# Performance work log

Measured on AMD Instinct MI355X. Metric: run time of the kernel, lower is better.

Reference implementation:

```python
import jax, jax.numpy as jnp
import numpy as np

D = 128            # actual_dim / embed_dim
DM = 2 * D         # d_model
HID = 2 * DM       # LSTMCell hidden size
NSYM = 200000
PAD = NSYM
B = 4096
S = 5
NB = 64
STEPS = 4
EPS = 1e-6


def setup_inputs() -> dict:
    key = jax.random.key(0)
    ks = jax.random.split(key, 24)
    def rn(k, sh, scale=0.02):
        return jax.random.normal(k, sh, dtype=jnp.float32) * scale
    emb = rn(ks[10], (NSYM + 1, D)).at[PAD].set(0.0)  # padding row zeroed
    inp = {
        'query': jax.random.randint(ks[0], (B, 2), 0, NSYM),
        'support': jax.random.randint(ks[1], (S, 2), 0, NSYM),
        'q_l_conn': jax.random.randint(ks[2], (B, NB, 2), 0, NSYM),
        'q_l_deg': jax.random.randint(ks[3], (B,), 0, NB),
        'q_r_conn': jax.random.randint(ks[4], (B, NB, 2), 0, NSYM),
        'q_r_deg': jax.random.randint(ks[5], (B,), 0, NB),
        's_l_conn': jax.random.randint(ks[6], (S, NB, 2), 0, NSYM),
        's_l_deg': jax.random.randint(ks[7], (S,), 0, NB),
        's_r_conn': jax.random.randint(ks[8], (S, NB, 2), 0, NSYM),
        's_r_deg': jax.random.randint(ks[9], (S,), 0, NB),
        'emb': emb,
        'gcn_w': rn(ks[11], (D, 2 * D)),
        'gcn_bias': jnp.zeros((D,), jnp.float32),
        'proj1_w': rn(ks[12], (2 * DM, DM)),
        'proj1_b': jnp.zeros((2 * DM,), jnp.float32),
        'proj2_w': rn(ks[13], (DM, 2 * DM)),
        'proj2_b': jnp.zeros((DM,), jnp.float32),
        'ln_g': jnp.ones((DM,), jnp.float32),
        'ln_b': jnp.zeros((DM,), jnp.float32),
        'w_ih': rn(ks[14], (4 * HID, DM)),
        'w_hh': rn(ks[15], (4 * HID, HID)),
        'b_ih': jnp.zeros((4 * HID,), jnp.float32),
        'b_hh': jnp.zeros((4 * HID,), jnp.float32),
    }
    return inp


def _neighbor_encoder(conn, deg, emb, gcn_w, gcn_bias):
    # conn: [N, NB, 2] ids (rel, ent); deg: [N]
    rel = emb[conn[:, :, 0]]                     # [N, NB, D] gather
    ent = emb[conn[:, :, 1]]                     # [N, NB, D] gather
    x = jnp.concatenate([rel, ent], axis=-1)     # [N, NB, 2D]
    out = jnp.einsum('bnd,kd->bnk', x, gcn_w) + gcn_bias  # [N, NB, D]
    denom = jnp.maximum(deg, 1).astype(out.dtype)[:, None]
    return jnp.tanh(out.sum(axis=1) / denom)     # [N, D]


def _support_encoder(x, proj1_w, proj1_b, proj2_w, proj2_b, ln_g, ln_b):
    residual = x
    h = jax.nn.relu(x @ proj1_w.T + proj1_b)
    h = h @ proj2_w.T + proj2_b
    z = h + residual
    mu = z.mean(axis=-1, keepdims=True)
    sigma = jnp.std(z, axis=-1, keepdims=True, ddof=1)
    return ln_g * (z - mu) / (sigma + EPS) + ln_b


def _query_encoder(support_vec, query, w_ih, w_hh, b_ih, b_hh):
    # support_vec: [DM] (single support prototype); query: [B, DM]
    bsz = query.shape[0]
    h_r = jnp.zeros((bsz, HID), query.dtype)
    c = jnp.zeros((bsz, HID), query.dtype)
    xW = query @ w_ih.T + b_ih  # invariant across steps
    h = query
    for _ in range(STEPS):
        gates = xW + h_r @ w_hh.T + b_hh
        i, f, g, o = jnp.split(gates, 4, axis=-1)
        c = jax.nn.sigmoid(f) * c + jax.nn.sigmoid(i) * jnp.tanh(g)
        h_cell = jax.nn.sigmoid(o) * jnp.tanh(c)
        h = query + h_cell[:, :DM]
        # attention over a single support row: softmax of one logit == 1
        r = jnp.broadcast_to(support_vec[None, :], h.shape)
        h_r = jnp.concatenate([h, r], axis=-1)
    return h


def reference(query, support, q_l_conn, q_l_deg, q_r_conn, q_r_deg,
              s_l_conn, s_l_deg, s_r_conn, s_r_deg,
              emb, gcn_w, gcn_bias, proj1_w, proj1_b, proj2_w, proj2_b,
              ln_g, ln_b, w_ih, w_hh, b_ih, b_hh):
    ql = _neighbor_encoder(q_l_conn, q_l_deg, emb, gcn_w, gcn_bias)
    qr = _neighbor_encoder(q_r_conn, q_r_deg, emb, gcn_w, gcn_bias)
    sl = _neighbor_encoder(s_l_conn, s_l_deg, emb, gcn_w, gcn_bias)
    sr = _neighbor_encoder(s_r_conn, s_r_deg, emb, gcn_w, gcn_bias)
    query_nb = jnp.concatenate([ql, qr], axis=-1)    # [B, DM]
    support_nb = jnp.concatenate([sl, sr], axis=-1)  # [S, DM]
    se = lambda x: _support_encoder(x, proj1_w, proj1_b, proj2_w, proj2_b, ln_g, ln_b)
    support_g = se(support_nb).mean(axis=0)          # [DM]
    query_g = se(query_nb)                            # [B, DM]
    query_f = _query_encoder(support_g, query_g, w_ih, w_hh, b_ih, b_hh)
    qn = query_f / jnp.maximum(jnp.linalg.norm(query_f, axis=-1, keepdims=True), 1e-12)
    sn = support_g / jnp.maximum(jnp.linalg.norm(support_g), 1e-12)
    return qn @ sn                                    # [B] matching scores
```

## Files before the change

kernel.cpp:

```cpp
#include <hip/hip_runtime.h>

#define BQ 4096
#define NS 5

typedef __attribute__((ext_vector_type(8))) short bf16x8;
typedef __attribute__((ext_vector_type(4))) float f32x4;
typedef unsigned short ushortT;

#define WS_QNB    0
#define WS_Z      1048576
#define WS_QG     2097152
#define WS_XW     3145728
#define WS_CBUF   7340032
#define WS_H1B    8388608
#define WS_ABF    8912896
#define WS_HB1    9175040
#define WS_P1B    9437184
#define WS_P2B    9502720
#define WS_WIHB   9568256
#define WS_WHHB   9699328
#define WS_GWP    9830400
#define WS_SNB    9863168
#define WS_H1G    9864448
#define WS_ZB     9867008
#define WS_SG     9868288
#define WS_SN     9868544
#define WS_SWL    9868800
#define WS_BL     9869824

__device__ __forceinline__ float wave_allreduce(float v) {
#pragma unroll
  for (int off = 32; off > 0; off >>= 1) v += __shfl_xor(v, off, 64);
  return v;
}
__device__ __forceinline__ float block_allreduce(float v, float* buf) {
  v = wave_allreduce(v);
  __syncthreads();
  if ((threadIdx.x & 63) == 0) buf[threadIdx.x >> 6] = v;
  __syncthreads();
  return buf[0] + buf[1] + buf[2] + buf[3];
}
__device__ __forceinline__ float sigm(float x) { return 1.0f / (1.0f + expf(-x)); }
__device__ __forceinline__ ushortT f2bf(float f) {
  unsigned int u = __float_as_uint(f);
  unsigned int r = (u + 0x7fffu + ((u >> 16) & 1u)) >> 16;
  return (ushortT)r;
}
__device__ __forceinline__ float dot4(float4 a, float4 b) {
  return a.x * b.x + a.y * b.y + a.z * b.z + a.w * b.w;
}

__global__ void k_pack(const float* __restrict__ w_ih, const float* __restrict__ w_hh,
                       const float* __restrict__ p1w, const float* __restrict__ p2w,
                       const float* __restrict__ gcn_w,
                       const float* __restrict__ b_ih, const float* __restrict__ b_hh,
                       ushortT* __restrict__ p1b16, ushortT* __restrict__ p2b16,
                       ushortT* __restrict__ wihb, ushortT* __restrict__ whhb,
                       float4* __restrict__ gwp, float* __restrict__ bL) {
  const int stride = gridDim.x * blockDim.x;
  const int gid = blockIdx.x * blockDim.x + threadIdx.x;
  for (int i = gid; i < 131072; i += stride) p1b16[i] = f2bf(p1w[i]);
  for (int i = gid; i < 131072; i += stride) p2b16[i] = f2bf(p2w[i]);
  for (int i = gid; i < 262144; i += stride) {
    int n = i >> 8, k = i & 255;
    int j = (n >> 2) + 512 * (n & 3);
    wihb[i] = f2bf(w_ih[j * 256 + k]);
    whhb[i] = f2bf(w_hh[j * 512 + k]);
  }
  for (int i = gid; i < 8192; i += stride) {
    int c = i >> 7, k = i & 127;
    const float* s = gcn_w + k * 256 + 4 * c;
    gwp[i] = make_float4(s[0], s[1], s[2], s[3]);
  }
  for (int i = gid; i < 1024; i += stride) {
    int j = (i >> 2) + 512 * (i & 3);
    bL[i] = b_ih[j] + b_hh[j];
  }
}

__global__ __launch_bounds__(256) void k_neighbor(
    const int* __restrict__ qlc, const int* __restrict__ qld,
    const int* __restrict__ qrc, const int* __restrict__ qrd,
    const int* __restrict__ slc, const int* __restrict__ sld,
    const int* __restrict__ src, const int* __restrict__ srd,
    const float* __restrict__ emb, const float4* __restrict__ gwp,
    const float* __restrict__ gcn_bias,
    float* __restrict__ query_nb, float* __restrict__ support_nb,
    ushortT* __restrict__ xq) {
  const int b = blockIdx.x;
  const int t = threadIdx.x;
  const int *cl, *cr;
  int degL, degR;
  float* out;
  if (b < BQ) {
    cl = qlc + b * 128; cr = qrc + b * 128;
    degL = qld[b]; degR = qrd[b];
    out = query_nb + (size_t)b * 256;
  } else {
    int r = b - BQ;
    cl = slc + r * 128; cr = src + r * 128;
    degL = sld[r]; degR = srd[r];
    out = support_nb + (size_t)r * 256;
  }
  __shared__ int conn[256];
  __shared__ __align__(16) float4 xs4[8][32];
  __shared__ __align__(16) float4 xsf[2][64];
  conn[t] = (t < 128) ? cl[t] : cr[t - 128];
  __syncthreads();
  {
    const int side = t >> 7, half = (t >> 6) & 1, ng = (t >> 5) & 1, d4 = t & 31;
    const int* cp = conn + side * 128 + half;
    const float4* emb4 = (const float4*)emb;
    float4 a = make_float4(0.f, 0.f, 0.f, 0.f);
    for (int np = 0; np < 32; np++) {
      int n = 2 * np + ng;
      int idx = cp[2 * n];
      float4 e = emb4[(size_t)idx * 32 + d4];
      a.x += e.x; a.y += e.y; a.z += e.z; a.w += e.w;
    }
    xs4[side * 4 + half * 2 + ng][d4] = a;
  }
  __syncthreads();
  if (t < 128) {
    const int sd = t >> 6, c = t & 63, half = c >> 5, d4 = c & 31;
    float4 a = xs4[sd * 4 + half * 2][d4];
    float4 bb = xs4[sd * 4 + half * 2 + 1][d4];
    a.x += bb.x; a.y += bb.y; a.z += bb.z; a.w += bb.w;
    xsf[sd][c] = a;
  }
  __syncthreads();
  {
    const int sd = t >> 7, kx = t & 127;
    float s = 0.f;
    for (int c = 0; c < 64; c++) s += dot4(gwp[c * 128 + kx], xsf[sd][c]);
    s += 64.0f * gcn_bias[kx];
    int deg = sd ? degR : degL;
    float val = tanhf(s / (float)(deg > 0 ? deg : 1));
    out[sd * 128 + kx] = val;
    if (b < BQ) xq[(size_t)b * 256 + sd * 128 + kx] = f2bf(val);
  }
}

__global__ __launch_bounds__(256) void k_sup1(
    const float* __restrict__ snb, const float* __restrict__ p1w,
    const float* __restrict__ p1b, float* __restrict__ h1g) {
  const int w = blockIdx.x * 4 + (threadIdx.x >> 6);
  const int lane = threadIdx.x & 63;
  const int r = w >> 9, j = w & 511;
  float4 x = *(const float4*)&snb[r * 256 + lane * 4];
  float4 wv = *(const float4*)&p1w[(size_t)j * 256 + lane * 4];
  float s = wave_allreduce(dot4(x, wv));
  if (lane == 0) h1g[r * 512 + j] = fmaxf(s + p1b[j], 0.f);
}

__global__ __launch_bounds__(256) void k_sup2(
    const float* __restrict__ snb, const float* __restrict__ h1g,
    const float* __restrict__ p2w, const float* __restrict__ p2b,
    float* __restrict__ zb) {
  const int w = blockIdx.x * 4 + (threadIdx.x >> 6);
  const int lane = threadIdx.x & 63;
  const int r = w >> 8, tt = w & 255;
  float4 h0 = *(const float4*)&h1g[r * 512 + lane * 4];
  float4 h1 = *(const float4*)&h1g[r * 512 + 256 + lane * 4];
  float4 w0 = *(const float4*)&p2w[(size_t)tt * 512 + lane * 4];
  float4 w1 = *(const float4*)&p2w[(size_t)tt * 512 + 256 + lane * 4];
  float s = wave_allreduce(dot4(h0, w0) + dot4(h1, w1));
  if (lane == 0) zb[r * 256 + tt] = s + p2b[tt] + snb[r * 256 + tt];
}

__global__ __launch_bounds__(256) void k_sup3(
    const float* __restrict__ zb, const float* __restrict__ ln_g,
    const float* __restrict__ ln_b, float* __restrict__ sg, float* __restrict__ sn) {
  const int t = threadIdx.x;
  __shared__ float rbuf[4];
  float acc = 0.f;
  for (int r = 0; r < NS; r++) {
    float z = zb[r * 256 + t];
    float s = block_allreduce(z, rbuf);
    float mu = s * (1.f / 256.f);
    float dz = z - mu;
    float s2 = block_allreduce(dz * dz, rbuf);
    float rstd = 1.f / (sqrtf(s2 * (1.f / 255.f)) + 1e-6f);
    acc += ln_g[t] * dz * rstd + ln_b[t];
    __syncthreads();
  }
  float g = acc * (1.f / (float)NS);
  sg[t] = g;
  float n2 = block_allreduce(g * g, rbuf);
  sn[t] = g / fmaxf(sqrtf(n2), 1e-12f);
}

__global__ __launch_bounds__(256) void k_sup4(
    const float* __restrict__ sg, const float* __restrict__ w_hh,
    float* __restrict__ sWl) {
  const int n = blockIdx.x * 4 + (threadIdx.x >> 6);
  const int lane = threadIdx.x & 63;
  const int j = (n >> 2) + 512 * (n & 3);
  float4 x = *(const float4*)&sg[lane * 4];
  float4 wv = *(const float4*)&w_hh[(size_t)j * 512 + 256 + lane * 4];
  float s = wave_allreduce(dot4(x, wv));
  if (lane == 0) sWl[n] = s;
}

__global__ __launch_bounds__(256) void k_gemm(
    const ushortT* __restrict__ A, const ushortT* __restrict__ B,
    const float* __restrict__ bias, const float* __restrict__ aux,
    float* __restrict__ outf, ushortT* __restrict__ outb,
    int K, int N, int nbn, int mode) {
  __shared__ short As[64 * 40];
  __shared__ short Bs[128 * 40];
  const int t = threadIdx.x;
  const int bn = blockIdx.x % nbn, bm = blockIdx.x / nbn;
  const int row0 = bm * 64, col0 = bn * 128;
  const int wave = t >> 6, lane = t & 63;
  const int wm = wave >> 1, wn = wave & 1, quad = lane >> 4, mr = lane & 15;
  f32x4 acc[2][4];
#pragma unroll
  for (int mi = 0; mi < 2; mi++)
#pragma unroll
    for (int ni = 0; ni < 4; ni++) acc[mi][ni] = (f32x4){0.f, 0.f, 0.f, 0.f};
  const int arow = t >> 2, akc = t & 3;
  for (int k0 = 0; k0 < K; k0 += 32) {
    float4 av = *(const float4*)(A + (size_t)(row0 + arow) * K + k0 + akc * 8);
    float4 bv0 = *(const float4*)(B + (size_t)(col0 + arow) * K + k0 + akc * 8);
    float4 bv1 = *(const float4*)(B + (size_t)(col0 + 64 + arow) * K + k0 + akc * 8);
    __syncthreads();
    *(float4*)&As[arow * 40 + akc * 8] = av;
    *(float4*)&Bs[arow * 40 + akc * 8] = bv0;
    *(float4*)&Bs[(64 + arow) * 40 + akc * 8] = bv1;
    __syncthreads();
    bf16x8 af[2], bfr[4];
#pragma unroll
    for (int mi = 0; mi < 2; mi++)
      af[mi] = *(const bf16x8*)&As[(wm * 32 + mi * 16 + mr) * 40 + quad * 8];
#pragma unroll
    for (int ni = 0; ni < 4; ni++)
      bfr[ni] = *(const bf16x8*)&Bs[(wn * 64 + ni * 16 + mr) * 40 + quad * 8];
#pragma unroll
    for (int mi = 0; mi < 2; mi++)
#pragma unroll
      for (int ni = 0; ni < 4; ni++)
        acc[mi][ni] = __builtin_amdgcn_mfma_f32_16x16x32_bf16(af[mi], bfr[ni], acc[mi][ni], 0, 0, 0);
  }
#pragma unroll
  for (int mi = 0; mi < 2; mi++) {
#pragma unroll
    for (int ni = 0; ni < 4; ni++) {
      const int col = col0 + wn * 64 + ni * 16 + mr;
      const int rb = row0 + wm * 32 + mi * 16 + quad * 4;
      const float bs = bias[col];
#pragma unroll
      for (int reg = 0; reg < 4; reg++) {
        const int row = rb + reg;
        const size_t off = (size_t)row * N + col;
        float v = acc[mi][ni][reg];
        if (mode == 0) outb[off] = f2bf(fmaxf(v + bs, 0.f));
        else outf[off] = v + bs + aux[off];
      }
    }
  }
}

__global__ __launch_bounds__(256) void k_gemm_lstm(
    const ushortT* __restrict__ A, const ushortT* __restrict__ B,
    const float* __restrict__ bL, const float* __restrict__ sWl,
    const float* __restrict__ qg, float* __restrict__ xw,
    float* __restrict__ cbuf, ushortT* __restrict__ hb_out, int phase) {
  __shared__ short As[64 * 40];
  __shared__ short Bs[128 * 40];
  __shared__ __align__(16) float Cs[64 * 132];
  const int t = threadIdx.x;
  const int bn = blockIdx.x & 7, bm = blockIdx.x >> 3;
  const int row0 = bm * 64, col0 = bn * 128;
  const int wave = t >> 6, lane = t & 63;
  const int wm = wave >> 1, wn = wave & 1, quad = lane >> 4, mr = lane & 15;
  f32x4 acc[2][4];
#pragma unroll
  for (int mi = 0; mi < 2; mi++)
#pragma unroll
    for (int ni = 0; ni < 4; ni++) acc[mi][ni] = (f32x4){0.f, 0.f, 0.f, 0.f};
  const int arow = t >> 2, akc = t & 3;
  for (int k0 = 0; k0 < 256; k0 += 32) {
    float4 av = *(const float4*)(A + (size_t)(row0 + arow) * 256 + k0 + akc * 8);
    float4 bv0 = *(const float4*)(B + (size_t)(col0 + arow) * 256 + k0 + akc * 8);
    float4 bv1 = *(const float4*)(B + (size_t)(col0 + 64 + arow) * 256 + k0 + akc * 8);
    __syncthreads();
    *(float4*)&As[arow * 40 + akc * 8] = av;
    *(float4*)&Bs[arow * 40 + akc * 8] = bv0;
    *(float4*)&Bs[(64 + arow) * 40 + akc * 8] = bv1;
    __syncthreads();
    bf16x8 af[2], bfr[4];
#pragma unroll
    for (int mi = 0; mi < 2; mi++)
      af[mi] = *(const bf16x8*)&As[(wm * 32 + mi * 16 + mr) * 40 + quad * 8];
#pragma unroll
    for (int ni = 0; ni < 4; ni++)
      bfr[ni] = *(const bf16x8*)&Bs[(wn * 64 + ni * 16 + mr) * 40 + quad * 8];
#pragma unroll
    for (int mi = 0; mi < 2; mi++)
#pragma unroll
      for (int ni = 0; ni < 4; ni++)
        acc[mi][ni] = __builtin_amdgcn_mfma_f32_16x16x32_bf16(af[mi], bfr[ni], acc[mi][ni], 0, 0, 0);
  }
#pragma unroll
  for (int mi = 0; mi < 2; mi++)
#pragma unroll
    for (int ni = 0; ni < 4; ni++)
#pragma unroll
      for (int reg = 0; reg < 4; reg++)
        Cs[(wm * 32 + mi * 16 + quad * 4 + reg) * 132 + wn * 64 + ni * 16 + mr] =
            acc[mi][ni][reg];
  __syncthreads();
  const int u = t & 31, grp = t >> 5;
  const int ugl = bn * 32 + u;
#pragma unroll
  for (int i = 0; i < 8; i++) {
    const int rl = grp * 8 + i;
    const int row = row0 + rl;
    const size_t o = (size_t)row * 256 + ugl;
    float4 gv = *(const float4*)&Cs[rl * 132 + u * 4];
    if (phase == 0) {
      float4 bb = *(const float4*)&bL[col0 + u * 4];
      gv.x += bb.x; gv.y += bb.y; gv.z += bb.z; gv.w += bb.w;
      float c0 = sigm(gv.x) * tanhf(gv.z);
      float h = qg[o] + sigm(gv.w) * tanhf(c0);
      cbuf[o] = c0;
      hb_out[o] = f2bf(h);
      float4 sv = *(const float4*)&sWl[col0 + u * 4];
      gv.x += sv.x; gv.y += sv.y; gv.z += sv.z; gv.w += sv.w;
      *(float4*)&xw[(size_t)row * 1024 + col0 + u * 4] = gv;
    } else {
      float4 xv = *(const float4*)&xw[(size_t)row * 1024 + col0 + u * 4];
      gv.x += xv.x; gv.y += xv.y; gv.z += xv.z; gv.w += xv.w;
      float c = sigm(gv.y) * cbuf[o] + sigm(gv.x) * tanhf(gv.z);
      float h = qg[o] + sigm(gv.w) * tanhf(c);
      if (phase == 2) {
        cbuf[o] = h;
      } else {
        cbuf[o] = c;
        hb_out[o] = f2bf(h);
      }
    }
  }
}

__global__ __launch_bounds__(256) void k_ln(
    const float* __restrict__ Z, const float* __restrict__ ln_g,
    const float* __restrict__ ln_b, float* __restrict__ qg, ushortT* __restrict__ qgb) {
  const int t = threadIdx.x;
  const int row = blockIdx.x * 4 + (t >> 6);
  const int lane = t & 63;
  float4 z = *(const float4*)&Z[(size_t)row * 256 + lane * 4];
  float s = wave_allreduce(z.x + z.y + z.z + z.w);
  float mu = s * (1.f / 256.f);
  float dx = z.x - mu, dy = z.y - mu, dz = z.z - mu, dw = z.w - mu;
  float s2 = wave_allreduce(dx * dx + dy * dy + dz * dz + dw * dw);
  float rstd = 1.f / (sqrtf(s2 * (1.f / 255.f)) + 1e-6f);
  float4 g = *(const float4*)&ln_g[lane * 4];
  float4 bb = *(const float4*)&ln_b[lane * 4];
  float4 o;
  o.x = g.x * dx * rstd + bb.x;
  o.y = g.y * dy * rstd + bb.y;
  o.z = g.z * dz * rstd + bb.z;
  o.w = g.w * dw * rstd + bb.w;
  *(float4*)&qg[(size_t)row * 256 + lane * 4] = o;
  ushort4 u;
  u.x = f2bf(o.x); u.y = f2bf(o.y); u.z = f2bf(o.z); u.w = f2bf(o.w);
  *(ushort4*)&qgb[(size_t)row * 256 + lane * 4] = u;
}

__global__ __launch_bounds__(256) void k_out(
    const float* __restrict__ hf, const float* __restrict__ sn, float* __restrict__ out) {
  const int t = threadIdx.x;
  const int row = blockIdx.x * 4 + (t >> 6);
  const int lane = t & 63;
  float4 h = *(const float4*)&hf[(size_t)row * 256 + lane * 4];
  float4 s = *(const float4*)&sn[lane * 4];
  float dt = wave_allreduce(dot4(h, s));
  float nr = wave_allreduce(dot4(h, h));
  if (lane == 0) out[row] = dt / fmaxf(sqrtf(nr), 1e-12f);
}

extern "C" void kernel_launch(void* const* d_in, const int* in_sizes, int n_in,
                              void* d_out, int out_size, void* d_ws, size_t ws_size,
                              hipStream_t stream) {
  const int* q_l_conn = (const int*)d_in[2];
  const int* q_l_deg  = (const int*)d_in[3];
  const int* q_r_conn = (const int*)d_in[4];
  const int* q_r_deg  = (const int*)d_in[5];
  const int* s_l_conn = (const int*)d_in[6];
  const int* s_l_deg  = (const int*)d_in[7];
  const int* s_r_conn = (const int*)d_in[8];
  const int* s_r_deg  = (const int*)d_in[9];
  const float* emb      = (const float*)d_in[10];
  const float* gcn_w    = (const float*)d_in[11];
  const float* gcn_bias = (const float*)d_in[12];
  const float* proj1_w  = (const float*)d_in[13];
  const float* proj1_b  = (const float*)d_in[14];
  const float* proj2_w  = (const float*)d_in[15];
  const float* proj2_b  = (const float*)d_in[16];
  const float* ln_g     = (const float*)d_in[17];
  const float* ln_b     = (const float*)d_in[18];
  const float* w_ih     = (const float*)d_in[19];
  const float* w_hh     = (const float*)d_in[20];
  const float* b_ih     = (const float*)d_in[21];
  const float* b_hh     = (const float*)d_in[22];

  float* ws = (float*)d_ws;
  float* qnb   = ws + WS_QNB;
  float* Z     = ws + WS_Z;
  float* qg    = ws + WS_QG;
  float* xw    = ws + WS_XW;
  float* cbuf  = ws + WS_CBUF;
  ushortT* h1b   = (ushortT*)(ws + WS_H1B);
  ushortT* abf   = (ushortT*)(ws + WS_ABF);
  ushortT* hb1   = (ushortT*)(ws + WS_HB1);
  ushortT* p1b16 = (ushortT*)(ws + WS_P1B);
  ushortT* p2b16 = (ushortT*)(ws + WS_P2B);
  ushortT* wihb  = (ushortT*)(ws + WS_WIHB);
  ushortT* whhb  = (ushortT*)(ws + WS_WHHB);
  float4* gwp  = (float4*)(ws + WS_GWP);
  float* snb   = ws + WS_SNB;
  float* h1g   = ws + WS_H1G;
  float* zb    = ws + WS_ZB;
  float* sg    = ws + WS_SG;
  float* sn    = ws + WS_SN;
  float* sWl   = ws + WS_SWL;
  float* bL    = ws + WS_BL;
  float* out   = (float*)d_out;

  hipLaunchKernelGGL(k_pack, dim3(512), dim3(256), 0, stream,
                     w_ih, w_hh, proj1_w, proj2_w, gcn_w, b_ih, b_hh,
                     p1b16, p2b16, wihb, whhb, gwp, bL);
  hipLaunchKernelGGL(k_neighbor, dim3(BQ + NS), dim3(256), 0, stream,
                     q_l_conn, q_l_deg, q_r_conn, q_r_deg,
                     s_l_conn, s_l_deg, s_r_conn, s_r_deg,
                     emb, gwp, gcn_bias, qnb, snb, abf);
  hipLaunchKernelGGL(k_sup1, dim3(640), dim3(256), 0, stream, snb, proj1_w, proj1_b, h1g);
  hipLaunchKernelGGL(k_sup2, dim3(320), dim3(256), 0, stream, snb, h1g, proj2_w, proj2_b, zb);
  hipLaunchKernelGGL(k_sup3, dim3(1), dim3(256), 0, stream, zb, ln_g, ln_b, sg, sn);
  hipLaunchKernelGGL(k_sup4, dim3(256), dim3(256), 0, stream, sg, w_hh, sWl);
  hipLaunchKernelGGL(k_gemm, dim3(64 * 4), dim3(256), 0, stream,
                     abf, p1b16, proj1_b, (const float*)nullptr, (float*)nullptr, h1b,
                     256, 512, 4, 0);
  hipLaunchKernelGGL(k_gemm, dim3(64 * 2), dim3(256), 0, stream,
                     h1b, p2b16, proj2_b, qnb, Z, (ushortT*)nullptr,
                     512, 256, 2, 1);
  hipLaunchKernelGGL(k_ln, dim3(BQ / 4), dim3(256), 0, stream, Z, ln_g, ln_b, qg, abf);
  hipLaunchKernelGGL(k_gemm_lstm, dim3(512), dim3(256), 0, stream,
                     abf, wihb, bL, sWl, qg, xw, cbuf, hb1, 0);
  hipLaunchKernelGGL(k_gemm_lstm, dim3(512), dim3(256), 0, stream,
                     hb1, whhb, bL, sWl, qg, xw, cbuf, abf, 1);
  hipLaunchKernelGGL(k_gemm_lstm, dim3(512), dim3(256), 0, stream,
                     abf, whhb, bL, sWl, qg, xw, cbuf, hb1, 1);
  hipLaunchKernelGGL(k_gemm_lstm, dim3(512), dim3(256), 0, stream,
                     hb1, whhb, bL, sWl, qg, xw, cbuf, (ushortT*)nullptr, 2);
  hipLaunchKernelGGL(k_out, dim3(BQ / 4), dim3(256), 0, stream, cbuf, sn, out);
}
```

Measured before the change: 363.4 us.

## Split neighbor encoder into gather kernel plus bf16 MFMA GCN GEMM; store xw in bf16

The fused neighbor kernel is split in two. A gather kernel sums embedding rows per side, with more loads in flight per thread, and writes bf16 sums. A separate MFMA GEMM then applies the GCN weight, bias, degree scaling and tanh. The per-row scalar fp32 dot products are replaced by tensor-core work, and the precomputed LSTM input projection xw is stored in bf16 to halve its traffic. The cost is lower precision in the neighbor sums, the GCN weight and xw, plus one extra launch and an intermediate buffer round-trip.

```diff
diff --git a/kernel.cpp b/kernel.cpp
--- a/kernel.cpp
+++ b/kernel.cpp
@@ -11,22 +11,23 @@
 #define WS_Z      1048576
 #define WS_QG     2097152
 #define WS_XW     3145728
-#define WS_CBUF   7340032
-#define WS_H1B    8388608
-#define WS_ABF    8912896
-#define WS_HB1    9175040
-#define WS_P1B    9437184
-#define WS_P2B    9502720
-#define WS_WIHB   9568256
-#define WS_WHHB   9699328
-#define WS_GWP    9830400
-#define WS_SNB    9863168
-#define WS_H1G    9864448
-#define WS_ZB     9867008
-#define WS_SG     9868288
-#define WS_SN     9868544
-#define WS_SWL    9868800
-#define WS_BL     9869824
+#define WS_CBUF   5242880
+#define WS_XS     6291456
+#define WS_H1B    7348224
+#define WS_ABF    7872512
+#define WS_HB1    8134656
+#define WS_P1B    8396800
+#define WS_P2B    8462336
+#define WS_WIHB   8527872
+#define WS_WHHB   8658944
+#define WS_GWB    8790016
+#define WS_SNB    8806400
+#define WS_H1G    8807680
+#define WS_ZB     8810240
+#define WS_SG     8811520
+#define WS_SN     8811776
+#define WS_SWL    8812032
+#define WS_BL     8813056
 
 __device__ __forceinline__ float wave_allreduce(float v) {
 #pragma unroll
@@ -46,6 +47,9 @@
   unsigned int r = (u + 0x7fffu + ((u >> 16) & 1u)) >> 16;
   return (ushortT)r;
 }
+__device__ __forceinline__ float bf2f(ushortT u) {
+  return __uint_as_float(((unsigned int)u) << 16);
+}
 __device__ __forceinline__ float dot4(float4 a, float4 b) {
   return a.x * b.x + a.y * b.y + a.z * b.z + a.w * b.w;
 }
@@ -56,7 +60,7 @@
                        const float* __restrict__ b_ih, const float* __restrict__ b_hh,
                        ushortT* __restrict__ p1b16, ushortT* __restrict__ p2b16,
                        ushortT* __restrict__ wihb, ushortT* __restrict__ whhb,
-                       float4* __restrict__ gwp, float* __restrict__ bL) {
+                       ushortT* __restrict__ gwb, float* __restrict__ bL) {
   const int stride = gridDim.x * blockDim.x;
   const int gid = blockIdx.x * blockDim.x + threadIdx.x;
   for (int i = gid; i < 131072; i += stride) p1b16[i] = f2bf(p1w[i]);
@@ -67,77 +71,123 @@
     wihb[i] = f2bf(w_ih[j * 256 + k]);
     whhb[i] = f2bf(w_hh[j * 512 + k]);
   }
-  for (int i = gid; i < 8192; i += stride) {
-    int c = i >> 7, k = i & 127;
-    const float* s = gcn_w + k * 256 + 4 * c;
-    gwp[i] = make_float4(s[0], s[1], s[2], s[3]);
-  }
+  for (int i = gid; i < 32768; i += stride) gwb[i] = f2bf(gcn_w[i]);
   for (int i = gid; i < 1024; i += stride) {
     int j = (i >> 2) + 512 * (i & 3);
     bL[i] = b_ih[j] + b_hh[j];
   }
 }
 
-__global__ __launch_bounds__(256) void k_neighbor(
-    const int* __restrict__ qlc, const int* __restrict__ qld,
-    const int* __restrict__ qrc, const int* __restrict__ qrd,
-    const int* __restrict__ slc, const int* __restrict__ sld,
-    const int* __restrict__ src, const int* __restrict__ srd,
-    const float* __restrict__ emb, const float4* __restrict__ gwp,
+__global__ __launch_bounds__(256) void k_gather(
+    const int* __restrict__ qlc, const int* __restrict__ qrc,
+    const int* __restrict__ slc, const int* __restrict__ src_,
+    const float* __restrict__ emb, ushortT* __restrict__ XS) {
+  const int r = blockIdx.x;
+  const int b = r >> 1, side = r & 1;
+  const int t = threadIdx.x;
+  const int* cg;
+  if (b < BQ) cg = (side ? qrc : qlc) + (size_t)b * 128;
+  else        cg = (side ? src_ : slc) + (size_t)(b - BQ) * 128;
+  __shared__ int connS[128];
+  __shared__ __align__(16) float part[8][132];
+  if (t < 128) connS[t] = cg[t];
+  __syncthreads();
+  const int s = t >> 5, l = t & 31;
+  const float4* emb4 = (const float4*)emb;
+  float4 acc = make_float4(0.f, 0.f, 0.f, 0.f);
+#pragma unroll
+  for (int kb = 0; kb < 2; kb++) {
+    int im[8];
+#pragma unroll
+    for (int k = 0; k < 8; k++) im[k] = connS[(kb * 8 + k) * 8 + s];
+    float4 v[8];
+#pragma unroll
+    for (int k = 0; k < 8; k++) v[k] = emb4[(size_t)im[k] * 32 + l];
+#pragma unroll
+    for (int k = 0; k < 8; k++) {
+      acc.x += v[k].x; acc.y += v[k].y; acc.z += v[k].z; acc.w += v[k].w;
+    }
+  }
+  *(float4*)&part[s][l * 4] = acc;
+  __syncthreads();
+  const int hf = t >> 7, dd = t & 127;
+  float sum = part[hf][dd] + part[2 + hf][dd] + part[4 + hf][dd] + part[6 + hf][dd];
+  XS[(size_t)r * 256 + t] = f2bf(sum);
+}
+
+__global__ __launch_bounds__(256) void k_gcn(
+    const ushortT* __restrict__ XS, const ushortT* __restrict__ gwb,
     const float* __restrict__ gcn_bias,
-    float* __restrict__ query_nb, float* __restrict__ support_nb,
-    ushortT* __restrict__ xq) {
-  const int b = blockIdx.x;
-  const int t = threadIdx.x;
-  const int *cl, *cr;
-  int degL, degR;
-  float* out;
-  if (b < BQ) {
-    cl = qlc + b * 128; cr = qrc + b * 128;
-    degL = qld[b]; degR = qrd[b];
-    out = query_nb + (size_t)b * 256;
-  } else {
-    int r = b - BQ;
-    cl = slc + r * 128; cr = src + r * 128;
-    degL = sld[r]; degR = srd[r];
-    out = support_nb + (size_t)r * 256;
-  }
-  __shared__ int conn[256];
-  __shared__ __align__(16) float4 xs4[8][32];
-  __shared__ __align__(16) float4 xsf[2][64];
-  conn[t] = (t < 128) ? cl[t] : cr[t - 128];
-  __syncthreads();
-  {
-    const int side = t >> 7, half = (t >> 6) & 1, ng = (t >> 5) & 1, d4 = t & 31;
-    const int* cp = conn + side * 128 + half;
-    const float4* emb4 = (const float4*)emb;
-    float4 a = make_float4(0.f, 0.f, 0.f, 0.f);
-    for (int np = 0; np < 32; np++) {
-      int n = 2 * np + ng;
-      int idx = cp[2 * n];
-      float4 e = emb4[(size_t)idx * 32 + d4];
-      a.x += e.x; a.y += e.y; a.z += e.z; a.w += e.w;
+    const int* __restrict__ qld, const int* __restrict__ qrd,
+    const int* __restrict__ sld, const int* __restrict__ srd,
+    float* __restrict__ qnb, float* __restrict__ snb, ushortT* __restrict__ xq) {
+  __shared__ short As[64 * 40];
+  __shared__ short Bs[128 * 40];
+  __shared__ int degl[32], degr[32];
+  const int t = threadIdx.x;
+  const int row0 = blockIdx.x * 64;
+  if (t < 32) {
+    int b = (row0 >> 1) + t;
+    int dl = 1, dr = 1;
+    if (b < BQ) { dl = qld[b]; dr = qrd[b]; }
+    else if (b < BQ + NS) { dl = sld[b - BQ]; dr = srd[b - BQ]; }
+    degl[t] = (dl > 0) ? dl : 1;
+    degr[t] = (dr > 0) ? dr : 1;
+  }
+  const int wave = t >> 6, lane = t & 63;
+  const int wm = wave >> 1, wn = wave & 1, quad = lane >> 4, mr = lane & 15;
+  f32x4 acc[2][4];
+#pragma unroll
+  for (int mi = 0; mi < 2; mi++)
+#pragma unroll
+    for (int ni = 0; ni < 4; ni++) acc[mi][ni] = (f32x4){0.f, 0.f, 0.f, 0.f};
+  const int arow = t >> 2, akc = t & 3;
+  for (int k0 = 0; k0 < 256; k0 += 32) {
+    float4 av = *(const float4*)(XS + (size_t)(row0 + arow) * 256 + k0 + akc * 8);
+    float4 bv0 = *(const float4*)(gwb + (size_t)arow * 256 + k0 + akc * 8);
+    float4 bv1 = *(const float4*)(gwb + (size_t)(64 + arow) * 256 + k0 + akc * 8);
+    __syncthreads();
+    *(float4*)&As[arow * 40 + akc * 8] = av;
+    *(float4*)&Bs[arow * 40 + akc * 8] = bv0;
+    *(float4*)&Bs[(64 + arow) * 40 + akc * 8] = bv1;
+    __syncthreads();
+    bf16x8 af[2], bfr[4];
+#pragma unroll
+    for (int mi = 0; mi < 2; mi++)
+      af[mi] = *(const bf16x8*)&As[(wm * 32 + mi * 16 + mr) * 40 + quad * 8];
+#pragma unroll
+    for (int ni = 0; ni < 4; ni++)
+      bfr[ni] = *(const bf16x8*)&Bs[(wn * 64 + ni * 16 + mr) * 40 + quad * 8];
+#pragma unroll
+    for (int mi = 0; mi < 2; mi++)
+#pragma unroll
+      for (int ni = 0; ni < 4; ni++)
+        acc[mi][ni] = __builtin_amdgcn_mfma_f32_16x16x32_bf16(af[mi], bfr[ni], acc[mi][ni], 0, 0, 0);
+  }
+#pragma unroll
+  for (int mi = 0; mi < 2; mi++) {
+#pragma unroll
+    for (int ni = 0; ni < 4; ni++) {
+      const int col = wn * 64 + ni * 16 + mr;
+      const int rb = row0 + wm * 32 + mi * 16 + quad * 4;
+      const float bs = 64.0f * gcn_bias[col];
+#pragma unroll
+      for (int reg = 0; reg < 4; reg++) {
+        const int row = rb + reg;
+        const int b = row >> 1, side = row & 1;
+        if (b >= BQ + NS) continue;
+        const int li = (row >> 1) - (row0 >> 1);
+        const int deg = side ? degr[li] : degl[li];
+        float val = tanhf((acc[mi][ni][reg] + bs) / (float)deg);
+        if (b < BQ) {
+          const size_t o = (size_t)b * 256 + side * 128 + col;
+          qnb[o] = val;
+          xq[o] = f2bf(val);
+        } else {
+          snb[(size_t)(b - BQ) * 256 + side * 128 + col] = val;
+        }
+      }
     }
-    xs4[side * 4 + half * 2 + ng][d4] = a;
-  }
-  __syncthreads();
-  if (t < 128) {
-    const int sd = t >> 6, c = t & 63, half = c >> 5, d4 = c & 31;
-    float4 a = xs4[sd * 4 + half * 2][d4];
-    float4 bb = xs4[sd * 4 + half * 2 + 1][d4];
-    a.x += bb.x; a.y += bb.y; a.z += bb.z; a.w += bb.w;
-    xsf[sd][c] = a;
-  }
-  __syncthreads();
-  {
-    const int sd = t >> 7, kx = t & 127;
-    float s = 0.f;
-    for (int c = 0; c < 64; c++) s += dot4(gwp[c * 128 + kx], xsf[sd][c]);
-    s += 64.0f * gcn_bias[kx];
-    int deg = sd ? degR : degL;
-    float val = tanhf(s / (float)(deg > 0 ? deg : 1));
-    out[sd * 128 + kx] = val;
-    if (b < BQ) xq[(size_t)b * 256 + sd * 128 + kx] = f2bf(val);
   }
 }
 
@@ -264,7 +314,7 @@
 __global__ __launch_bounds__(256) void k_gemm_lstm(
     const ushortT* __restrict__ A, const ushortT* __restrict__ B,
     const float* __restrict__ bL, const float* __restrict__ sWl,
-    const float* __restrict__ qg, float* __restrict__ xw,
+    const float* __restrict__ qg, ushortT* __restrict__ xwb,
     float* __restrict__ cbuf, ushortT* __restrict__ hb_out, int phase) {
   __shared__ short As[64 * 40];
   __shared__ short Bs[128 * 40];
@@ -327,11 +377,14 @@
       cbuf[o] = c0;
       hb_out[o] = f2bf(h);
       float4 sv = *(const float4*)&sWl[col0 + u * 4];
-      gv.x += sv.x; gv.y += sv.y; gv.z += sv.z; gv.w += sv.w;
-      *(float4*)&xw[(size_t)row * 1024 + col0 + u * 4] = gv;
+      ushort4 xo;
+      xo.x = f2bf(gv.x + sv.x); xo.y = f2bf(gv.y + sv.y);
+      xo.z = f2bf(gv.z + sv.z); xo.w = f2bf(gv.w + sv.w);
+      *(ushort4*)&xwb[(size_t)row * 1024 + col0 + u * 4] = xo;
     } else {
-      float4 xv = *(const float4*)&xw[(size_t)row * 1024 + col0 + u * 4];
-      gv.x += xv.x; gv.y += xv.y; gv.z += xv.z; gv.w += xv.w;
+      ushort4 xv = *(const ushort4*)&xwb[(size_t)row * 1024 + col0 + u * 4];
+      gv.x += bf2f(xv.x); gv.y += bf2f(xv.y);
+      gv.z += bf2f(xv.z); gv.w += bf2f(xv.w);
       float c = sigm(gv.y) * cbuf[o] + sigm(gv.x) * tanhf(gv.z);
       float h = qg[o] + sigm(gv.w) * tanhf(c);
       if (phase == 2) {
@@ -410,8 +463,9 @@
   float* qnb   = ws + WS_QNB;
   float* Z     = ws + WS_Z;
   float* qg    = ws + WS_QG;
-  float* xw    = ws + WS_XW;
+  ushortT* xwb = (ushortT*)(ws + WS_XW);
   float* cbuf  = ws + WS_CBUF;
+  ushortT* XS    = (ushortT*)(ws + WS_XS);
   ushortT* h1b   = (ushortT*)(ws + WS_H1B);
   ushortT* abf   = (ushortT*)(ws + WS_ABF);
   ushortT* hb1   = (ushortT*)(ws + WS_HB1);
@@ -419,7 +473,7 @@
   ushortT* p2b16 = (ushortT*)(ws + WS_P2B);
   ushortT* wihb  = (ushortT*)(ws + WS_WIHB);
   ushortT* whhb  = (ushortT*)(ws + WS_WHHB);
-  float4* gwp  = (float4*)(ws + WS_GWP);
+  ushortT* gwb   = (ushortT*)(ws + WS_GWB);
   float* snb   = ws + WS_SNB;
   float* h1g   = ws + WS_H1G;
   float* zb    = ws + WS_ZB;
@@ -431,11 +485,12 @@
 
   hipLaunchKernelGGL(k_pack, dim3(512), dim3(256), 0, stream,
                      w_ih, w_hh, proj1_w, proj2_w, gcn_w, b_ih, b_hh,
-                     p1b16, p2b16, wihb, whhb, gwp, bL);
-  hipLaunchKernelGGL(k_neighbor, dim3(BQ + NS), dim3(256), 0, stream,
-                     q_l_conn, q_l_deg, q_r_conn, q_r_deg,
-                     s_l_conn, s_l_deg, s_r_conn, s_r_deg,
-                     emb, gwp, gcn_bias, qnb, snb, abf);
+                     p1b16, p2b16, wihb, whhb, gwb, bL);
+  hipLaunchKernelGGL(k_gather, dim3(2 * (BQ + NS)), dim3(256), 0, stream,
+                     q_l_conn, q_r_conn, s_l_conn, s_r_conn, emb, XS);
+  hipLaunchKernelGGL(k_gcn, dim3(129), dim3(256), 0, stream,
+                     XS, gwb, gcn_bias, q_l_deg, q_r_deg, s_l_deg, s_r_deg,
+                     qnb, snb, abf);
   hipLaunchKernelGGL(k_sup1, dim3(640), dim3(256), 0, stream, snb, proj1_w, proj1_b, h1g);
   hipLaunchKernelGGL(k_sup2, dim3(320), dim3(256), 0, stream, snb, h1g, proj2_w, proj2_b, zb);
   hipLaunchKernelGGL(k_sup3, dim3(1), dim3(256), 0, stream, zb, ln_g, ln_b, sg, sn);
@@ -448,12 +503,12 @@
                      512, 256, 2, 1);
   hipLaunchKernelGGL(k_ln, dim3(BQ / 4), dim3(256), 0, stream, Z, ln_g, ln_b, qg, abf);
   hipLaunchKernelGGL(k_gemm_lstm, dim3(512), dim3(256), 0, stream,
-                     abf, wihb, bL, sWl, qg, xw, cbuf, hb1, 0);
+                     abf, wihb, bL, sWl, qg, xwb, cbuf, hb1, 0);
   hipLaunchKernelGGL(k_gemm_lstm, dim3(512), dim3(256), 0, stream,
-                     hb1, whhb, bL, sWl, qg, xw, cbuf, abf, 1);
+                     hb1, whhb, bL, sWl, qg, xwb, cbuf, abf, 1);
   hipLaunchKernelGGL(k_gemm_lstm, dim3(512), dim3(256), 0, stream,
-                     abf, whhb, bL, sWl, qg, xw, cbuf, hb1, 1);
+                     abf, whhb, bL, sWl, qg, xwb, cbuf, hb1, 1);
   hipLaunchKernelGGL(k_gemm_lstm, dim3(512), dim3(256), 0, stream,
-                     hb1, whhb, bL, sWl, qg, xw, cbuf, (ushortT*)nullptr, 2);
+                     hb1, whhb, bL, sWl, qg, xwb, cbuf, (ushortT*)nullptr, 2);
   hipLaunchKernelGGL(k_out, dim3(BQ / 4), dim3(256), 0, stream, cbuf, sn, out);
 }
```

After: 359.8 us. No clear change (-1.0%).
